# Performance work log

Measured on AMD Instinct MI355X. Metric: run time of the kernel, lower is better.

The kernel has to match this reference:

```python
import jax, jax.numpy as jnp
import numpy as np
from jax import lax

B, C, H, W = 16, 128, 64, 64
O, K, KS = 128, 4, 3
R = max(C // 4, 1)  # reduced channels in SE branch


def setup_inputs() -> dict:
    key = jax.random.key(0)
    ks = jax.random.split(key, 6)
    x = jax.random.normal(ks[0], (B, C, H, W), dtype=jnp.float32)
    # SE-style weight generator: 1x1 convs == linears on pooled features
    w1 = jax.random.normal(ks[1], (R, C), dtype=jnp.float32) * (1.0 / np.sqrt(C))
    b1 = jnp.zeros((R,), dtype=jnp.float32)
    w2 = jax.random.normal(ks[2], (K, R), dtype=jnp.float32) * (1.0 / np.sqrt(R))
    b2 = jnp.zeros((K,), dtype=jnp.float32)
    # bank of conv kernels, torch init is randn
    kernels = jax.random.normal(ks[3], (K, O, C, KS, KS), dtype=jnp.float32)
    return {"x": x, "w1": w1, "b1": b1, "w2": w2, "b2": b2, "kernels": kernels}


def reference(x, w1, b1, w2, b2, kernels):
    b = x.shape[0]
    # --- attention over kernels (SE branch) ---
    pooled = jnp.mean(x, axis=(2, 3))                    # (B, C)
    h = jax.nn.relu(pooled @ w1.T + b1)                  # (B, R)
    attn = jax.nn.softmax(h @ w2.T + b2, axis=1)         # (B, K)
    # --- all K convolutions fused into one conv with K*O output channels ---
    k, o, c, kh, kw = kernels.shape
    wflat = kernels.reshape(k * o, c, kh, kw)
    pad = (kh - 1) // 2
    conv = lax.conv_general_dilated(
        x, wflat,
        window_strides=(1, 1),
        padding=[(pad, pad), (pad, pad)],
        dimension_numbers=("NCHW", "OIHW", "NCHW"),
    )                                                    # (B, K*O, H, W)
    conv = conv.reshape(b, k, o, conv.shape[2], conv.shape[3])
    # per-sample weighted sum over the kernel bank
    out = jnp.einsum("bk,bkohw->bohw", attn, conv)       # (B, O, H, W)
    return out
```

## Files before the change

### kernel.cpp

```cpp
#include <hip/hip_runtime.h>


#define BB 16
#define CC 128
#define HH 64
#define WW 64
#define OO 128
#define KK 4
#define RR 32
#define KTOT 1152
#define NT 36
#define XP 66

typedef short v8s __attribute__((ext_vector_type(8)));
typedef float v4f __attribute__((ext_vector_type(4)));

__device__ __forceinline__ unsigned short f2bf(float f) {
    unsigned u = __builtin_bit_cast(unsigned, f);
    u += 0x7fffu + ((u >> 16) & 1u);
    return (unsigned short)(u >> 16);
}

__device__ __forceinline__ void gl16(const unsigned short* g, unsigned short* l) {
    __builtin_amdgcn_global_load_lds(
        (const __attribute__((address_space(1))) unsigned int*)g,
        (__attribute__((address_space(3))) unsigned int*)l, 16, 0, 0);
}

__global__ __launch_bounds__(256) void convert_pool_kernel(const float* __restrict__ x,
        unsigned short* __restrict__ xbp, float* __restrict__ part) {
    int bid = blockIdx.x;
    int t = threadIdx.x;
    int p = (bid & 15) * 256 + t;
    int g = (bid >> 4) & 15;
    int b = bid >> 8;
    const float* xp = x + ((size_t)(b * CC + g * 8)) * 4096 + p;
    float vals[8];
    v8s v;
    #pragma unroll
    for (int j = 0; j < 8; ++j) {
        vals[j] = xp[(size_t)j * 4096];
        v[j] = (short)f2bf(vals[j]);
    }
    int h = p >> 6, w = p & 63;
    unsigned short* xb_b = xbp + (size_t)b * XP * XP * CC + g * 8;
    *(v8s*)(xb_b + (size_t)((h + 1) * XP + w + 1) * CC) = v;

    v8s z = (v8s)0;
    if (w == 0)  *(v8s*)(xb_b + (size_t)((h + 1) * XP) * CC) = z;
    if (w == 63) *(v8s*)(xb_b + (size_t)((h + 1) * XP + 65) * CC) = z;
    if (h == 0)  *(v8s*)(xb_b + (size_t)(w + 1) * CC) = z;
    if (h == 63) *(v8s*)(xb_b + (size_t)(65 * XP + w + 1) * CC) = z;
    if (h == 0 && w == 0)   *(v8s*)(xb_b + 0) = z;
    if (h == 0 && w == 63)  *(v8s*)(xb_b + (size_t)65 * CC) = z;
    if (h == 63 && w == 0)  *(v8s*)(xb_b + (size_t)(65 * XP) * CC) = z;
    if (h == 63 && w == 63) *(v8s*)(xb_b + (size_t)(65 * XP + 65) * CC) = z;

    __shared__ float ls[4][8];
    int lane = t & 63, wv = t >> 6;
    #pragma unroll
    for (int j = 0; j < 8; ++j) {
        float s = vals[j];
        #pragma unroll
        for (int off = 32; off > 0; off >>= 1) s += __shfl_down(s, off, 64);
        if (lane == 0) ls[wv][j] = s;
    }
    __syncthreads();
    if (t < 8) {
        float s = ls[0][t] + ls[1][t] + ls[2][t] + ls[3][t];
        part[(((b * 16 + g) * 16) + (bid & 15)) * 8 + t] = s;
    }
}

__global__ __launch_bounds__(256) void mix_kernel(const float* __restrict__ kernels,
        const float* __restrict__ part,
        const float* __restrict__ w1, const float* __restrict__ b1,
        const float* __restrict__ w2, const float* __restrict__ b2,
        unsigned short* __restrict__ wmixb) {
    const int b = blockIdx.y, o = blockIdx.x;
    const int t = threadIdx.x;
    __shared__ float pooled_sh[CC];
    __shared__ float hs[RR];
    __shared__ float lgs[KK];
    __shared__ float attns[KK];
    __shared__ unsigned short ws[KTOT];

    if (t < CC) {
        const float* pp = part + ((b * 16 + (t >> 3)) * 16) * 8 + (t & 7);
        float s = 0.f;
        #pragma unroll
        for (int pb = 0; pb < 16; ++pb) s += pp[pb * 8];
        pooled_sh[t] = s * (1.0f / 4096.0f);
    }
    __syncthreads();
    if (t < RR) {
        float acc = b1[t];
        const float* wr = w1 + t * CC;
        for (int c = 0; c < CC; ++c) acc += pooled_sh[c] * wr[c];
        hs[t] = fmaxf(acc, 0.f);
    }
    __syncthreads();
    if (t < KK) {
        float a = b2[t];
        #pragma unroll
        for (int r = 0; r < RR; ++r) a += hs[r] * w2[t * RR + r];
        lgs[t] = a;
    }
    __syncthreads();
    if (t == 0) {
        float m = fmaxf(fmaxf(lgs[0], lgs[1]), fmaxf(lgs[2], lgs[3]));
        float e0 = expf(lgs[0] - m), e1 = expf(lgs[1] - m);
        float e2 = expf(lgs[2] - m), e3 = expf(lgs[3] - m);
        float inv = 1.f / (e0 + e1 + e2 + e3);
        attns[0] = e0 * inv; attns[1] = e1 * inv; attns[2] = e2 * inv; attns[3] = e3 * inv;
    }
    __syncthreads();
    float a0 = attns[0], a1 = attns[1], a2 = attns[2], a3 = attns[3];

    const size_t KB = (size_t)OO * KTOT;
    const float* k0 = kernels + (size_t)o * KTOT;
    for (int ii = t; ii < KTOT; ii += 256) {
        int c = ii / 9, tap = ii - c * 9;
        float v = a0 * k0[ii] + a1 * k0[KB + ii] + a2 * k0[2 * KB + ii] + a3 * k0[3 * KB + ii];
        ws[tap * 128 + c] = f2bf(v);
    }
    __syncthreads();
    v8s* wp8 = (v8s*)(wmixb + ((size_t)b * OO + o) * KTOT);
    const v8s* ls8 = (const v8s*)ws;
    for (int ii = t; ii < KTOT / 8; ii += 256) wp8[ii] = ls8[ii];
}

#define MFMA16(acc, va, vb) \
    asm volatile("v_mfma_f32_16x16x32_bf16 %0, %1, %2, %0" : "+v"(acc) : "v"(va), "v"(vb))

#define STAGE(ks_, buf_) { \
    const int tap_ = (ks_) >> 2; \
    const int dy_ = tap_ / 3, dx_ = tap_ % 3; \
    const int c0_ = ((ks_) & 3) * 32; \
    const unsigned short* sa_ = srcA0 + (ks_) * 32; \
    const unsigned short* sb_ = srcB0 + ((size_t)(dy_ * XP + dx_)) * CC + c0_; \
    gl16(sa_,                     &Ab[buf_][wid * 512]); \
    gl16(sa_ + (size_t)64 * KTOT, &Ab[buf_][(wid + 4) * 512]); \
    gl16(sb_,                     &Bb[buf_][wid * 512]); \
    gl16(sb_ + XP * CC,           &Bb[buf_][(wid + 4) * 512]); \
}

__global__ __launch_bounds__(256, 2) void conv_kernel(
        const unsigned short* __restrict__ xbp,
        const unsigned short* __restrict__ wmixb,
        float* __restrict__ out) {
    __shared__ unsigned short Ab[3][4096];
    __shared__ unsigned short Bb[3][4096];
    int bid = blockIdx.x;
    int xcd = bid & 7, idx = bid >> 3;
    int b = xcd * 2 + (idx >> 5);
    int nt = idx & 31;
    int t = threadIdx.x;
    int lane = t & 63, wid = t >> 6;
    int wm = wid & 1, wn = wid >> 1;

    v4f acc[4][4];
    #pragma unroll
    for (int i = 0; i < 4; ++i)
        #pragma unroll
        for (int j = 0; j < 4; ++j) acc[i][j] = (v4f)0.f;

    int l4 = lane >> 2, g = lane & 3;
    const unsigned short* srcA0 = wmixb + ((size_t)(b * OO + wid * 16 + l4)) * KTOT + g * 8;
    const unsigned short* srcB0 = xbp + ((size_t)((b * XP + nt * 2) * XP) + wid * 16 + l4) * CC + g * 8;
    int lane_off = (lane & 15) * 64 + (lane >> 4) * 16;

    STAGE(0, 0);
    STAGE(1, 1);

    #pragma unroll
    for (int ks = 0; ks < NT; ++ks) {
        if (ks == NT - 1) {
            asm volatile("s_waitcnt vmcnt(0)" ::: "memory");
        } else {
            asm volatile("s_waitcnt vmcnt(4)" ::: "memory");
        }
        __builtin_amdgcn_s_barrier();
        if (ks + 2 < NT) STAGE(ks + 2, (ks + 2) % 3);
        const int buf_ = ks % 3;
        v8s af[4], bfv[4];
        const char* abase = (const char*)&Ab[buf_][0] + wm * 4096 + lane_off;
        const char* bbase = (const char*)&Bb[buf_][0] + wn * 4096 + lane_off;
        #pragma unroll
        for (int mf = 0; mf < 4; ++mf) af[mf] = *(const v8s*)(abase + mf * 1024);
        #pragma unroll
        for (int nf = 0; nf < 4; ++nf) bfv[nf] = *(const v8s*)(bbase + nf * 1024);
        #pragma unroll
        for (int mf = 0; mf < 4; ++mf)
            #pragma unroll
            for (int nf = 0; nf < 4; ++nf)
                MFMA16(acc[mf][nf], af[mf], bfv[nf]);
    }
    asm volatile("s_nop 7\ns_nop 7" ::: );

    int r = nt * 2 + wn;
    #pragma unroll
    for (int mf = 0; mf < 4; ++mf) {
        int o = wm * 64 + mf * 16 + ((lane >> 4) << 2);
        #pragma unroll
        for (int jj = 0; jj < 4; ++jj) {
            float* op = out + (((size_t)(b * OO + o + jj)) * HH + r) * WW;
            #pragma unroll
            for (int nf = 0; nf < 4; ++nf)
                op[nf * 16 + (lane & 15)] = acc[mf][nf][jj];
        }
    }
}

extern "C" void kernel_launch(void* const* d_in, const int* in_sizes, int n_in,
                              void* d_out, int out_size, void* d_ws, size_t ws_size,
                              hipStream_t stream) {
    const float* x       = (const float*)d_in[0];
    const float* w1      = (const float*)d_in[1];
    const float* b1      = (const float*)d_in[2];
    const float* w2      = (const float*)d_in[3];
    const float* b2      = (const float*)d_in[4];
    const float* kernels = (const float*)d_in[5];
    float* out = (float*)d_out;

    float* part = (float*)d_ws;
    unsigned short* xbp   = (unsigned short*)(part + 16 * 16 * 16 * 8);
    unsigned short* wmixb = xbp + (size_t)BB * XP * XP * CC;

    convert_pool_kernel<<<4096, 256, 0, stream>>>(x, xbp, part);
    mix_kernel<<<dim3(OO, BB), 256, 0, stream>>>(kernels, part, w1, b1, w2, b2, wmixb);
    conv_kernel<<<512, 256, 0, stream>>>(xbp, wmixb, out);
}
```

Before: 58.87 us.

## Restructure convert/pool kernel to transpose whole rows through shared memory

The NCHW-to-padded-NHWC bf16 conversion now gives each block one image row across all 128 channels. Data is staged in an LDS tile so global writes become full 16-byte contiguous channel chunks, replacing the earlier scattered 8-channel writes. Padding is written cooperatively, and the pooling partials are reorganized per row, so the mix kernel's reduction now sums 64 partials per channel. The goal is better write coalescing and fewer blocks; the cost is 32 loads per thread, more shuffle reductions and fewer blocks for latency hiding.

```diff
diff --git a/kernel.cpp b/kernel.cpp
--- a/kernel.cpp
+++ b/kernel.cpp
@@ -29,46 +29,49 @@
 
 __global__ __launch_bounds__(256) void convert_pool_kernel(const float* __restrict__ x,
         unsigned short* __restrict__ xbp, float* __restrict__ part) {
-    int bid = blockIdx.x;
+    int b = blockIdx.y, s = blockIdx.x;
     int t = threadIdx.x;
-    int p = (bid & 15) * 256 + t;
-    int g = (bid >> 4) & 15;
-    int b = bid >> 8;
-    const float* xp = x + ((size_t)(b * CC + g * 8)) * 4096 + p;
-    float vals[8];
-    v8s v;
-    #pragma unroll
-    for (int j = 0; j < 8; ++j) {
-        vals[j] = xp[(size_t)j * 4096];
-        v[j] = (short)f2bf(vals[j]);
-    }
-    int h = p >> 6, w = p & 63;
-    unsigned short* xb_b = xbp + (size_t)b * XP * XP * CC + g * 8;
-    *(v8s*)(xb_b + (size_t)((h + 1) * XP + w + 1) * CC) = v;
-
+    int px = t & 63, cg = t >> 6;
+    __shared__ unsigned short xt[64][130];
+
+    const float* xpb = x + (size_t)b * CC * 4096 + s * 64 + px;
+    float v[32];
+    #pragma unroll
+    for (int j = 0; j < 32; ++j) {
+        v[j] = xpb[(size_t)(cg * 32 + j) * 4096];
+        xt[px][cg * 32 + j] = f2bf(v[j]);
+    }
+
+    unsigned short* xb_b = xbp + (size_t)b * XP * XP * CC;
     v8s z = (v8s)0;
-    if (w == 0)  *(v8s*)(xb_b + (size_t)((h + 1) * XP) * CC) = z;
-    if (w == 63) *(v8s*)(xb_b + (size_t)((h + 1) * XP + 65) * CC) = z;
-    if (h == 0)  *(v8s*)(xb_b + (size_t)(w + 1) * CC) = z;
-    if (h == 63) *(v8s*)(xb_b + (size_t)(65 * XP + w + 1) * CC) = z;
-    if (h == 0 && w == 0)   *(v8s*)(xb_b + 0) = z;
-    if (h == 0 && w == 63)  *(v8s*)(xb_b + (size_t)65 * CC) = z;
-    if (h == 63 && w == 0)  *(v8s*)(xb_b + (size_t)(65 * XP) * CC) = z;
-    if (h == 63 && w == 63) *(v8s*)(xb_b + (size_t)(65 * XP + 65) * CC) = z;
-
-    __shared__ float ls[4][8];
-    int lane = t & 63, wv = t >> 6;
-    #pragma unroll
-    for (int j = 0; j < 8; ++j) {
-        float s = vals[j];
-        #pragma unroll
-        for (int off = 32; off > 0; off >>= 1) s += __shfl_down(s, off, 64);
-        if (lane == 0) ls[wv][j] = s;
-    }
-    __syncthreads();
-    if (t < 8) {
-        float s = ls[0][t] + ls[1][t] + ls[2][t] + ls[3][t];
-        part[(((b * 16 + g) * 16) + (bid & 15)) * 8 + t] = s;
+    if (t >= 16 && t < 32) *(v8s*)(xb_b + (size_t)((s + 1) * XP + 0)  * CC + (t - 16) * 8) = z;
+    if (t >= 48 && t < 64) *(v8s*)(xb_b + (size_t)((s + 1) * XP + 65) * CC + (t - 48) * 8) = z;
+    if (s == 0) {
+        for (int e = t; e < 2112; e += 256) {
+            int cell = e >> 4, chunk = e & 15;
+            int row = (cell < 66) ? 0 : 65;
+            int col = (cell < 66) ? cell : cell - 66;
+            *(v8s*)(xb_b + (size_t)(row * XP + col) * CC + chunk * 8) = z;
+        }
+    }
+
+    #pragma unroll
+    for (int j = 0; j < 32; ++j) {
+        float sv = v[j];
+        #pragma unroll
+        for (int off = 32; off > 0; off >>= 1) sv += __shfl_down(sv, off, 64);
+        if (px == 0) part[((size_t)b * 64 + s) * CC + cg * 32 + j] = sv;
+    }
+    __syncthreads();
+
+    int chunk = t & 15, pxq = t >> 4;
+    #pragma unroll
+    for (int r = 0; r < 4; ++r) {
+        int p2 = r * 16 + pxq;
+        const unsigned int* lp = (const unsigned int*)&xt[p2][chunk * 8];
+        uint4 u;
+        u.x = lp[0]; u.y = lp[1]; u.z = lp[2]; u.w = lp[3];
+        *(uint4*)(xb_b + ((size_t)(s + 1) * XP + p2 + 1) * CC + chunk * 8) = u;
     }
 }
 
@@ -86,10 +89,10 @@
     __shared__ unsigned short ws[KTOT];
 
     if (t < CC) {
-        const float* pp = part + ((b * 16 + (t >> 3)) * 16) * 8 + (t & 7);
+        const float* pp = part + (size_t)b * 64 * CC + t;
         float s = 0.f;
         #pragma unroll
-        for (int pb = 0; pb < 16; ++pb) s += pp[pb * 8];
+        for (int sb = 0; sb < 64; ++sb) s += pp[sb * CC];
         pooled_sh[t] = s * (1.0f / 4096.0f);
     }
     __syncthreads();
@@ -224,10 +227,10 @@
     float* out = (float*)d_out;
 
     float* part = (float*)d_ws;
-    unsigned short* xbp   = (unsigned short*)(part + 16 * 16 * 16 * 8);
+    unsigned short* xbp   = (unsigned short*)(part + BB * 64 * CC);
     unsigned short* wmixb = xbp + (size_t)BB * XP * XP * CC;
 
-    convert_pool_kernel<<<4096, 256, 0, stream>>>(x, xbp, part);
+    convert_pool_kernel<<<dim3(64, BB), 256, 0, stream>>>(x, xbp, part);
     mix_kernel<<<dim3(OO, BB), 256, 0, stream>>>(kernels, part, w1, b1, w2, b2, wmixb);
     conv_kernel<<<512, 256, 0, stream>>>(xbp, wmixb, out);
 }
```

Result: slower. 63.87 us (+8.5%).
